# Kernel tuning notes

Hardware: AMD Instinct MI355X
Metric: run time of the kernel (lower is better)

Reference implementation:

```python
import jax, jax.numpy as jnp
import numpy as np

EPS = 1e-5

def _mesh_conv_point(f, nbr, w, b):
    # f: [B, C, V] features; nbr: [B, V, K] neighbor vertex indices
    # gather neighbor features per batch: [B, C, V, K]
    g = jax.vmap(lambda fb, nb: fb[:, nb])(f, nbr)
    # prepend self feature -> [B, C, V, K+1]
    x = jnp.concatenate([f[:, :, :, None], g], axis=3)
    # Conv2d with kernel (1, K+1) == contraction over (C, K+1)
    return jnp.einsum('bcvk,ock->bov', x, w) + b[None, :, None]

def _instance_norm(y):
    # InstanceNorm2d (affine=False): normalize over spatial dims (V, 1)
    m = jnp.mean(y, axis=2, keepdims=True)
    v = jnp.var(y, axis=2, keepdims=True)
    return (y - m) * jax.lax.rsqrt(v + EPS)

def setup_inputs() -> dict:
    key = jax.random.key(0)
    k1, k2, k3, k4 = jax.random.split(key, 4)
    B, Cin, Cout, V, K = 4, 64, 128, 50000, 6
    fe = jax.random.normal(k1, (B, Cin, V), dtype=jnp.float32)
    nbrs = jax.random.randint(k2, (B, V, K), 0, V, dtype=jnp.int32)
    w1 = jax.random.normal(k3, (Cout, Cin, K + 1), dtype=jnp.float32) * (1.0 / np.sqrt(Cin * (K + 1)))
    b1 = jnp.zeros((Cout,), dtype=jnp.float32)
    w2 = jax.random.normal(k4, (Cout, Cout, K + 1), dtype=jnp.float32) * (1.0 / np.sqrt(Cout * (K + 1)))
    b2 = jnp.zeros((Cout,), dtype=jnp.float32)
    return {"fe": fe, "nbrs": nbrs, "w1": w1, "b1": b1, "w2": w2, "b2": b2}

def reference(fe, nbrs, w1, b1, w2, b2):
    # conv1 -> instance norm -> relu
    x1 = jax.nn.relu(_instance_norm(_mesh_conv_point(fe, nbrs, w1, b1)))
    # residual block: conv2 -> instance norm -> + x1 -> relu
    x2 = jax.nn.relu(_instance_norm(_mesh_conv_point(x1, nbrs, w2, b2)) + x1)
    # pool=0, so output == before_pool; return the single [B, Cout, V] tensor
    return x2
```

## Files before the change

### kernel.cpp

```cpp
#include <hip/hip_runtime.h>
#include <cstdint>
#include <cstddef>
#include <utility>

typedef unsigned short u16;
typedef u16 u16x8 __attribute__((ext_vector_type(8)));
typedef u16 u16x4 __attribute__((ext_vector_type(4)));
typedef _Float16 f16x8 __attribute__((ext_vector_type(8)));
typedef float f32x4 __attribute__((ext_vector_type(4)));

constexpr int B    = 4;
constexpr int CIN  = 64;
constexpr int COUT = 128;
constexpr int V    = 50000;
constexpr int KP1  = 7;
constexpr float EPS = 1e-5f;

constexpr int BN   = 128;
constexpr int NT   = (V + BN - 1) / BN;
constexpr int NTP  = 392;
constexpr int NT64 = (V + 63) / 64;

__device__ __forceinline__ u16 f2h(float f) {
    _Float16 h = (_Float16)f;
    return __builtin_bit_cast(u16, h);
}
__device__ __forceinline__ float h2f(u16 s) {
    return (float)__builtin_bit_cast(_Float16, s);
}

template<int... Is, typename F>
__device__ __forceinline__ void static_for_impl(F&& f, std::integer_sequence<int, Is...>) {
    (f(std::integral_constant<int, Is>{}), ...);
}
template<int N, typename F>
__device__ __forceinline__ void static_for(F&& f) {
    static_for_impl(f, std::make_integer_sequence<int, N>{});
}

template<int C>
__global__ __launch_bounds__(256) void prep_wf(const float* __restrict__ w,
                                               u16* __restrict__ wF) {
    constexpr int RCH = KP1 * C / 32;
    const int g = blockIdx.x * 256 + threadIdx.x;
    if (g >= RCH * 8 * 64) return;
    const int l  = g & 63;
    const int m  = (g >> 6) & 7;
    const int ch = g >> 9;
    const int k  = ch / (C / 32);
    const int c0 = (ch % (C / 32)) * 32;
    const int o  = m * 16 + (l & 15);
    u16x8 out;
#pragma unroll
    for (int j = 0; j < 8; ++j) {
        const int c = c0 + (l >> 4) * 8 + j;
        out[j] = f2h(w[((size_t)o * C + c) * KP1 + k]);
    }
    *(u16x8*)&wF[(size_t)g * 8] = out;
}

__global__ __launch_bounds__(256) void transpose_fe(const float* __restrict__ fe,
                                                    u16* __restrict__ feT) {
    __shared__ u16 tile[32][33];
    const int t  = threadIdx.x;
    const int tx = t & 31, ty = t >> 5;
    const int v0 = blockIdx.x * 32;
    const int c0 = blockIdx.y * 32;
    const int b  = blockIdx.z;
#pragma unroll
    for (int p = 0; p < 4; ++p) {
        const int c = c0 + ty + p * 8;
        const int v = v0 + tx;
        if (v < V) tile[ty + p * 8][tx] = f2h(fe[((size_t)b * CIN + c) * V + v]);
    }
    __syncthreads();
#pragma unroll
    for (int p = 0; p < 4; ++p) {
        const int v = v0 + ty + p * 8;
        const int c = c0 + tx;
        if (v < V) feT[((size_t)b * V + v) * CIN + c] = tile[tx][ty + p * 8];
    }
}

template<int C, int INL, int OUTL>
__global__ __launch_bounds__(256, 3) void conv_mfma(const void* __restrict__ xin_,
                                                    const u16*  __restrict__ wF,
                                                    const float* __restrict__ bias,
                                                    const int*  __restrict__ nbr,
                                                    void* __restrict__ out_,
                                                    float2* __restrict__ P) {
    constexpr int RCH  = KP1 * C / 32;
    constexpr int KSH  = (C == 64) ? 1 : 2;
    constexpr int KMSK = (C / 32) - 1;
    __shared__ __align__(16) u16 Xl[3][BN][40];
    __shared__ float2 Sred[4][COUT];

    const int t    = threadIdx.x;
    const int b    = blockIdx.x / NT;
    const int tile = blockIdx.x % NT;
    const int v0   = tile * BN;
    const int w    = t >> 6;
    const int l    = t & 63;
    const int wo   = (w & 1) * 64;
    const int wv   = (w >> 1) * 64;
    const int seg  = (l >> 4) * 8;

    const int sv = t >> 1;
    const int hc = (t & 1) * 16;
    const int vS = v0 + sv;
    const bool okS = vS < V;
    int idxS[KP1];
    {
        const int vc = okS ? vS : 0;
        idxS[0] = vc;
#pragma unroll
        for (int k = 1; k < KP1; ++k)
            idxS[k] = nbr[((size_t)b * V + vc) * 6 + (k - 1)];
    }

    int vn[4]; bool ok[4];
#pragma unroll
    for (int n = 0; n < 4; ++n) {
        vn[n] = v0 + wv + n * 16 + (l & 15);
        ok[n] = vn[n] < V;
    }

    f32x4 acc[4][4];
#pragma unroll
    for (int m = 0; m < 4; ++m)
#pragma unroll
        for (int n = 0; n < 4; ++n) acc[m][n] = (f32x4)0.f;

    f16x8 af[2][4];
    u16x8 g[2][2];

    auto gload = [&](auto CHC, u16x8 (&gr)[2]) {
        constexpr int CH  = decltype(CHC)::value;
        constexpr int k_  = CH >> KSH;
        constexpr int c0_ = (CH & KMSK) * 32;
        if constexpr (INL == 0) {
            const u16* x_ = (const u16*)xin_;
            const u16* p_ = &x_[((size_t)b * V + idxS[k_]) * C + c0_ + hc];
            gr[0] = *(const u16x8*)(p_);
            gr[1] = *(const u16x8*)(p_ + 8);
        } else {
            const float* x_ = (const float*)xin_;
#pragma unroll
            for (int j = 0; j < 16; ++j) {
                const float v_ = x_[((size_t)b * C + c0_ + hc + j) * V + idxS[k_]];
                gr[j >> 3][j & 7] = f2h(v_);
            }
        }
    };
    auto aload = [&](auto CHC, f16x8 (&ar)[4]) {
        constexpr int CH = decltype(CHC)::value;
#pragma unroll
        for (int m = 0; m < 4; ++m)
            ar[m] = *(const f16x8*)&wF[(((size_t)CH * 8 + (wo >> 4) + m) * 64 + l) * 8];
    };

    gload(std::integral_constant<int, 0>{}, g[0]);
    gload(std::integral_constant<int, 1>{}, g[1]);
    aload(std::integral_constant<int, 0>{}, af[0]);
    *(u16x8*)&Xl[0][sv][hc]     = g[0][0];
    *(u16x8*)&Xl[0][sv][hc + 8] = g[0][1];
    asm volatile("s_waitcnt lgkmcnt(0)" ::: "memory");
    __builtin_amdgcn_s_barrier();

    static_for<RCH>([&](auto CHC) {
        constexpr int ch = decltype(CHC)::value;
        constexpr int rb = ch % 3;
        f16x8 bf[4];
#pragma unroll
        for (int n = 0; n < 4; ++n)
            bf[n] = *(const f16x8*)&Xl[rb][wv + n * 16 + (l & 15)][seg];
        if constexpr (ch + 1 < RCH) {
            aload(std::integral_constant<int, ch + 1>{}, af[(ch + 1) & 1]);
            constexpr int wb = (ch + 1) % 3;
            *(u16x8*)&Xl[wb][sv][hc]     = g[(ch + 1) & 1][0];
            *(u16x8*)&Xl[wb][sv][hc + 8] = g[(ch + 1) & 1][1];
        }
        if constexpr (ch + 2 < RCH)
            gload(std::integral_constant<int, ch + 2>{}, g[ch & 1]);
#pragma unroll
        for (int m = 0; m < 4; ++m)
#pragma unroll
            for (int n = 0; n < 4; ++n)
                acc[m][n] = __builtin_amdgcn_mfma_f32_16x16x32_f16(af[ch & 1][m], bf[n],
                                                                   acc[m][n], 0, 0, 0);
        if constexpr (ch + 1 < RCH) {
            asm volatile("s_waitcnt lgkmcnt(0)" ::: "memory");
            __builtin_amdgcn_s_barrier();
        }
    });

    if constexpr (OUTL == 0) {
        u16* po = (u16*)out_;
#pragma unroll
        for (int n = 0; n < 4; ++n) {
            if (ok[n]) {
#pragma unroll
                for (int m = 0; m < 4; ++m) {
                    const int o = wo + m * 16 + ((l >> 4) << 2);
                    u16x4 pk;
#pragma unroll
                    for (int q = 0; q < 4; ++q) pk[q] = f2h(acc[m][n][q] + bias[o + q]);
                    *(u16x4*)&po[((size_t)b * V + vn[n]) * COUT + o] = pk;
                }
            }
        }
    } else {
        float* po = (float*)out_;
#pragma unroll
        for (int m = 0; m < 4; ++m) {
            const int o = wo + m * 16 + ((l >> 4) << 2);
#pragma unroll
            for (int q = 0; q < 4; ++q) {
                const float bq = bias[o + q];
#pragma unroll
                for (int n = 0; n < 4; ++n)
                    if (ok[n]) po[((size_t)(b * COUT + o + q)) * V + vn[n]] = acc[m][n][q] + bq;
            }
        }
    }

#pragma unroll
    for (int m = 0; m < 4; ++m) {
        const int o = wo + m * 16 + ((l >> 4) << 2);
        float s[4], s2[4];
#pragma unroll
        for (int q = 0; q < 4; ++q) {
            const float bq = bias[o + q];
            float a = 0.f, aa = 0.f;
#pragma unroll
            for (int n = 0; n < 4; ++n) {
                if (ok[n]) {
                    const float val = acc[m][n][q] + bq;
                    a += val; aa += val * val;
                }
            }
            s[q] = a; s2[q] = aa;
        }
#pragma unroll
        for (int d = 1; d < 16; d <<= 1) {
#pragma unroll
            for (int q = 0; q < 4; ++q) {
                s[q]  += __shfl_xor(s[q],  d, 16);
                s2[q] += __shfl_xor(s2[q], d, 16);
            }
        }
        if ((l & 15) == 0) {
#pragma unroll
            for (int q = 0; q < 4; ++q)
                Sred[w][o + q] = make_float2(s[q], s2[q]);
        }
    }
    __syncthreads();
    if (t < COUT) {
        const int wlo = t >> 6;
        const float2 a = Sred[wlo][t];
        const float2 c = Sred[wlo + 2][t];
        P[((size_t)b * COUT + t) * NTP + tile] = make_float2(a.x + c.x, a.y + c.y);
    }
}

__global__ __launch_bounds__(256) void finalize_fused(const float2* __restrict__ P,
                                                      float2* __restrict__ S) {
    const int row = blockIdx.x;
    float s = 0.f, s2 = 0.f;
    for (int i = threadIdx.x; i < NT; i += 256) {
        const float2 p = P[(size_t)row * NTP + i];
        s += p.x; s2 += p.y;
    }
    __shared__ float2 red[256];
    red[threadIdx.x] = make_float2(s, s2);
    __syncthreads();
    for (int w = 128; w > 0; w >>= 1) {
        if (threadIdx.x < w) {
            red[threadIdx.x].x += red[threadIdx.x + w].x;
            red[threadIdx.x].y += red[threadIdx.x + w].y;
        }
        __syncthreads();
    }
    if (threadIdx.x == 0) {
        const float m = red[0].x / V;
        const float var = red[0].y / V - m * m;
        S[row] = make_float2(m, rsqrtf(var + EPS));
    }
}

__global__ __launch_bounds__(256) void norm1(u16* __restrict__ x,
                                             const float2* __restrict__ S) {
    const unsigned e = ((unsigned)blockIdx.x * 256u + threadIdx.x) * 8u;
    if (e >= (unsigned)B * V * COUT) return;
    const unsigned b  = e / ((unsigned)V * COUT);
    const unsigned o0 = e & 127u;
    u16x8 vv = *(u16x8*)&x[e];
#pragma unroll
    for (int j = 0; j < 8; ++j) {
        const float2 s = S[b * COUT + o0 + j];
        float f = (h2f(vv[j]) - s.x) * s.y;
        vv[j] = f2h(fmaxf(f, 0.f));
    }
    *(u16x8*)&x[e] = vv;
}

__global__ __launch_bounds__(256) void final_mix2(const u16* __restrict__ y2,
                                                  const u16* __restrict__ x1,
                                                  const float2* __restrict__ S,
                                                  float* __restrict__ out) {
    __shared__ float ty[64][33], tx[64][33];
    const int t  = threadIdx.x;
    const int v0 = blockIdx.x * 64;
    const int o0 = blockIdx.y * 32;
    const int b  = blockIdx.z;
    const int jr = (t & 7) * 4;
    const int ir = t >> 3;
#pragma unroll
    for (int p = 0; p < 2; ++p) {
        const int i = ir + p * 32;
        const int v = v0 + i;
        if (v < V) {
            const size_t base = ((size_t)b * V + v) * COUT + o0 + jr;
            const u16x4 a = *(const u16x4*)&y2[base];
            const u16x4 c = *(const u16x4*)&x1[base];
#pragma unroll
            for (int q = 0; q < 4; ++q) {
                ty[i][jr + q] = h2f(a[q]);
                tx[i][jr + q] = h2f(c[q]);
            }
        }
    }
    __syncthreads();
    const int vl = t & 63, v = v0 + vl, oo0 = t >> 6;
    if (v < V) {
#pragma unroll
        for (int p = 0; p < 8; ++p) {
            const int oo = oo0 + p * 4;
            const int o  = o0 + oo;
            const float2 s = S[b * COUT + o];
            out[((size_t)b * COUT + o) * V + v] =
                fmaxf((ty[vl][oo] - s.x) * s.y + tx[vl][oo], 0.f);
        }
    }
}

__global__ __launch_bounds__(256) void final_mix(float* __restrict__ y,
                                                 const u16* __restrict__ x1,
                                                 const float2* __restrict__ S) {
    __shared__ float tile[64][33];
    const int t  = threadIdx.x;
    const int v0 = blockIdx.x * 64;
    const int o0 = blockIdx.y * 32;
    const int b  = blockIdx.z;
    const int j  = t & 31;
    const int i0 = t >> 5;
#pragma unroll
    for (int p = 0; p < 8; ++p) {
        const int i = i0 + p * 8;
        const int v = v0 + i;
        tile[i][j] = (v < V) ? h2f(x1[((size_t)b * V + v) * COUT + o0 + j]) : 0.f;
    }
    __syncthreads();
    const int vl  = t & 63;
    const int v   = v0 + vl;
    const int oo0 = t >> 6;
    if (v < V) {
#pragma unroll
        for (int p = 0; p < 8; ++p) {
            const int oo = oo0 + p * 4;
            const int o  = o0 + oo;
            const size_t idx = ((size_t)b * COUT + o) * V + v;
            const float2 s = S[b * COUT + o];
            const float f = (y[idx] - s.x) * s.y + tile[vl][oo];
            y[idx] = fmaxf(f, 0.f);
        }
    }
}

extern "C" void kernel_launch(void* const* d_in, const int* in_sizes, int n_in,
                              void* d_out, int out_size, void* d_ws, size_t ws_size,
                              hipStream_t stream) {
    const float* fe  = (const float*)d_in[0];
    const int*   nbr = (const int*)d_in[1];
    const float* w1  = (const float*)d_in[2];
    const float* b1  = (const float*)d_in[3];
    const float* w2  = (const float*)d_in[4];
    const float* b2  = (const float*)d_in[5];
    float* outf = (float*)d_out;
    char*  ws   = (char*)d_ws;

    constexpr size_t wF1_b = (size_t)(KP1 * CIN  / 32) * 8 * 64 * 8 * 2;
    constexpr size_t wF2_b = (size_t)(KP1 * COUT / 32) * 8 * 64 * 8 * 2;
    constexpr size_t S_b   = (size_t)B * COUT * 8;
    constexpr size_t Pf_b  = (size_t)B * COUT * NTP * 8;
    constexpr size_t x1_b  = (size_t)B * V * COUT * 2;
    constexpr size_t y2_b  = (size_t)B * V * COUT * 2;
    constexpr size_t feT_b = (size_t)B * V * CIN * 2;
    const size_t base = wF1_b + wF2_b + 2 * S_b + Pf_b;

    const bool full = (ws_size >= base + x1_b + y2_b);
    const bool t3   = (ws_size >= base + x1_b + feT_b);
    const bool t4   = (ws_size >= base + x1_b);
    if (!full && !t3 && !t4) return;

    size_t off = 0;
    u16*    wF1 = (u16*)(ws + off);    off += wF1_b;
    u16*    wF2 = (u16*)(ws + off);    off += wF2_b;
    float2* S1  = (float2*)(ws + off); off += S_b;
    float2* S2  = (float2*)(ws + off); off += S_b;
    float2* P   = (float2*)(ws + off); off += Pf_b;
    u16*    x1  = (u16*)(ws + off);    off += x1_b;
    u16*    ext = (u16*)(ws + off);

    prep_wf<CIN> <<<(KP1 * CIN  / 32) * 8 * 64 / 256, 256, 0, stream>>>(w1, wF1);
    prep_wf<COUT><<<(KP1 * COUT / 32) * 8 * 64 / 256, 256, 0, stream>>>(w2, wF2);

    const bool useFeT = full || t3;
    if (useFeT) {
        dim3 gt((V + 31) / 32, CIN / 32, B);
        transpose_fe<<<gt, 256, 0, stream>>>(fe, ext);
    }

    if (useFeT) conv_mfma<CIN, 0, 0><<<B * NT, 256, 0, stream>>>(ext, wF1, b1, nbr, x1, P);
    else        conv_mfma<CIN, 1, 0><<<B * NT, 256, 0, stream>>>(fe,  wF1, b1, nbr, x1, P);
    finalize_fused<<<B * COUT, 256, 0, stream>>>(P, S1);
    norm1<<<(int)((size_t)B * V * COUT / 8 / 256), 256, 0, stream>>>(x1, S1);

    dim3 gf(NT64, COUT / 32, B);
    if (full) {
        u16* y2 = ext;
        conv_mfma<COUT, 0, 0><<<B * NT, 256, 0, stream>>>(x1, wF2, b2, nbr, y2, P);
        finalize_fused<<<B * COUT, 256, 0, stream>>>(P, S2);
        final_mix2<<<gf, 256, 0, stream>>>(y2, x1, S2, outf);
    } else {
        conv_mfma<COUT, 0, 1><<<B * NT, 256, 0, stream>>>(x1, wF2, b2, nbr, outf, P);
        finalize_fused<<<B * COUT, 256, 0, stream>>>(P, S2);
        final_mix<<<gf, 256, 0, stream>>>(outf, x1, S2);
    }
}
```

Measured before the change: 236.5 us.

## Widen conv K-step to 64 channels with double-buffered LDS staging

```diff
diff --git a/kernel.cpp b/kernel.cpp
--- a/kernel.cpp
+++ b/kernel.cpp
@@ -83,16 +83,14 @@
 }
 
 template<int C, int INL, int OUTL>
-__global__ __launch_bounds__(256, 3) void conv_mfma(const void* __restrict__ xin_,
+__global__ __launch_bounds__(256, 2) void conv_mfma(const void* __restrict__ xin_,
                                                     const u16*  __restrict__ wF,
                                                     const float* __restrict__ bias,
                                                     const int*  __restrict__ nbr,
                                                     void* __restrict__ out_,
                                                     float2* __restrict__ P) {
-    constexpr int RCH  = KP1 * C / 32;
-    constexpr int KSH  = (C == 64) ? 1 : 2;
-    constexpr int KMSK = (C / 32) - 1;
-    __shared__ __align__(16) u16 Xl[3][BN][40];
+    constexpr int NS = KP1 * C / 64;
+    __shared__ __align__(16) u16 Xl[2][BN][72];
     __shared__ float2 Sred[4][COUT];
 
     const int t    = threadIdx.x;
@@ -103,15 +101,13 @@
     const int l    = t & 63;
     const int wo   = (w & 1) * 64;
     const int wv   = (w >> 1) * 64;
-    const int seg  = (l >> 4) * 8;
 
     const int sv = t >> 1;
-    const int hc = (t & 1) * 16;
+    const int h  = t & 1;
     const int vS = v0 + sv;
-    const bool okS = vS < V;
     int idxS[KP1];
     {
-        const int vc = okS ? vS : 0;
+        const int vc = (vS < V) ? vS : 0;
         idxS[0] = vc;
 #pragma unroll
         for (int k = 1; k < KP1; ++k)
@@ -131,64 +127,74 @@
 #pragma unroll
         for (int n = 0; n < 4; ++n) acc[m][n] = (f32x4)0.f;
 
-    f16x8 af[2][4];
-    u16x8 g[2][2];
-
-    auto gload = [&](auto CHC, u16x8 (&gr)[2]) {
-        constexpr int CH  = decltype(CHC)::value;
-        constexpr int k_  = CH >> KSH;
-        constexpr int c0_ = (CH & KMSK) * 32;
+    u16x8 g[2][4];
+    f16x8 af[2][8];
+
+    auto gload = [&](auto SC, u16x8 (&gr)[4]) {
+        constexpr int S    = decltype(SC)::value;
+        constexpr int k_   = (C == 64) ? S : (S >> 1);
+        constexpr int off_ = (C == 64) ? 0 : (S & 1) * 64;
         if constexpr (INL == 0) {
             const u16* x_ = (const u16*)xin_;
-            const u16* p_ = &x_[((size_t)b * V + idxS[k_]) * C + c0_ + hc];
-            gr[0] = *(const u16x8*)(p_);
-            gr[1] = *(const u16x8*)(p_ + 8);
+            const u16* p_ = &x_[((size_t)b * V + idxS[k_]) * C + off_ + h * 32];
+#pragma unroll
+            for (int j = 0; j < 4; ++j) gr[j] = *(const u16x8*)(p_ + j * 8);
         } else {
             const float* x_ = (const float*)xin_;
 #pragma unroll
-            for (int j = 0; j < 16; ++j) {
-                const float v_ = x_[((size_t)b * C + c0_ + hc + j) * V + idxS[k_]];
+            for (int j = 0; j < 32; ++j) {
+                const float v_ = x_[((size_t)b * C + off_ + h * 32 + j) * V + idxS[k_]];
                 gr[j >> 3][j & 7] = f2h(v_);
             }
         }
     };
-    auto aload = [&](auto CHC, f16x8 (&ar)[4]) {
-        constexpr int CH = decltype(CHC)::value;
-#pragma unroll
-        for (int m = 0; m < 4; ++m)
-            ar[m] = *(const f16x8*)&wF[(((size_t)CH * 8 + (wo >> 4) + m) * 64 + l) * 8];
+    auto aload = [&](auto SC, f16x8 (&ar)[8]) {
+        constexpr int S = decltype(SC)::value;
+#pragma unroll
+        for (int kc = 0; kc < 2; ++kc)
+#pragma unroll
+            for (int m = 0; m < 4; ++m)
+                ar[kc * 4 + m] =
+                    *(const f16x8*)&wF[(((size_t)(2 * S + kc) * 8 + (wo >> 4) + m) * 64 + l) * 8];
     };
+    auto store = [&](int bufi, u16x8 (&gr)[4]) {
+#pragma unroll
+        for (int j = 0; j < 4; ++j)
+            *(u16x8*)&Xl[bufi][sv][h * 32 + j * 8] = gr[j];
+    };
 
     gload(std::integral_constant<int, 0>{}, g[0]);
-    gload(std::integral_constant<int, 1>{}, g[1]);
+    if constexpr (NS > 1) gload(std::integral_constant<int, 1>{}, g[1]);
     aload(std::integral_constant<int, 0>{}, af[0]);
-    *(u16x8*)&Xl[0][sv][hc]     = g[0][0];
-    *(u16x8*)&Xl[0][sv][hc + 8] = g[0][1];
+    store(0, g[0]);
     asm volatile("s_waitcnt lgkmcnt(0)" ::: "memory");
     __builtin_amdgcn_s_barrier();
 
-    static_for<RCH>([&](auto CHC) {
-        constexpr int ch = decltype(CHC)::value;
-        constexpr int rb = ch % 3;
-        f16x8 bf[4];
+    static_for<NS>([&](auto SC) {
+        constexpr int s = decltype(SC)::value;
+        f16x8 bf[4][2];
 #pragma unroll
         for (int n = 0; n < 4; ++n)
-            bf[n] = *(const f16x8*)&Xl[rb][wv + n * 16 + (l & 15)][seg];
-        if constexpr (ch + 1 < RCH) {
-            aload(std::integral_constant<int, ch + 1>{}, af[(ch + 1) & 1]);
-            constexpr int wb = (ch + 1) % 3;
-            *(u16x8*)&Xl[wb][sv][hc]     = g[(ch + 1) & 1][0];
-            *(u16x8*)&Xl[wb][sv][hc + 8] = g[(ch + 1) & 1][1];
-        }
-        if constexpr (ch + 2 < RCH)
-            gload(std::integral_constant<int, ch + 2>{}, g[ch & 1]);
-#pragma unroll
-        for (int m = 0; m < 4; ++m)
-#pragma unroll
-            for (int n = 0; n < 4; ++n)
-                acc[m][n] = __builtin_amdgcn_mfma_f32_16x16x32_f16(af[ch & 1][m], bf[n],
-                                                                   acc[m][n], 0, 0, 0);
-        if constexpr (ch + 1 < RCH) {
+#pragma unroll
+            for (int kc = 0; kc < 2; ++kc)
+                bf[n][kc] = *(const f16x8*)&Xl[s & 1][wv + n * 16 + (l & 15)]
+                                              [kc * 32 + (l >> 4) * 8];
+        if constexpr (s + 2 < NS)
+            gload(std::integral_constant<int, s + 2>{}, g[s & 1]);
+        if constexpr (s + 1 < NS)
+            aload(std::integral_constant<int, s + 1>{}, af[(s + 1) & 1]);
+#pragma unroll
+        for (int kc = 0; kc < 2; ++kc)
+#pragma unroll
+            for (int m = 0; m < 4; ++m)
+#pragma unroll
+                for (int n = 0; n < 4; ++n)
+                    acc[m][n] = __builtin_amdgcn_mfma_f32_16x16x32_f16(af[s & 1][kc * 4 + m],
+                                                                       bf[n][kc],
+                                                                       acc[m][n], 0, 0, 0);
+        if constexpr (s + 1 < NS) {
+            __builtin_amdgcn_sched_barrier(0);
+            store((s + 1) & 1, g[(s + 1) & 1]);
             asm volatile("s_waitcnt lgkmcnt(0)" ::: "memory");
             __builtin_amdgcn_s_barrier();
         }
```

After: 233.4 us. About the same (-1.3%).
